# Optimization experiments

Measured on AMD Instinct MI355X. Metric: run time of the kernel, lower is better.

Reference implementation:

```python
import jax, jax.numpy as jnp
import numpy as np

N_OUT = 4096
N_IN = 4096
FRAC_SPARSE = 0.5
N_SPARSE = int(FRAC_SPARSE * N_OUT * N_IN)  # 8388608
TOKENS = 256


def setup_inputs() -> dict:
    key = jax.random.key(0)
    k1, k2 = jax.random.split(key)
    # x: activations fed to F.linear
    x = jax.random.normal(k1, (TOKENS, N_IN), dtype=jnp.float32)
    # sparse_values: nn.Parameter of size n_sparse
    sparse_values = jax.random.normal(k2, (N_SPARSE,), dtype=jnp.float32) * 0.02
    # sparse_mask as sorted unique row-major flat indices of True entries.
    # torch `out[mask] = values` fills values into True positions in row-major
    # order, which equals scattering values at the ascending-sorted flat idxs.
    rng = np.random.default_rng(0)
    flat_idx = np.sort(rng.permutation(N_OUT * N_IN)[:N_SPARSE]).astype(np.int32)
    return {"x": x, "sparse_values": sparse_values, "flat_idx": jnp.asarray(flat_idx)}


def reference(x, sparse_values, flat_idx):
    # reconstruct(): dense [n_out, n_in] weight via scatter of sparse values
    W = (
        jnp.zeros((N_OUT * N_IN,), dtype=sparse_values.dtype)
        .at[flat_idx]
        .set(sparse_values)
        .reshape(N_OUT, N_IN)
    )
    # F.linear(x, W) == x @ W.T
    return x @ W.T
```

## Files before the change

### kernel.cpp

```cpp
#include <hip/hip_runtime.h>
#include <stdint.h>

#define N_OUT    4096
#define N_IN     4096
#define TOKENS   256
#define N_SPARSE 8388608
#define SPLITK   8
#define KCHUNK   256
#define NCHUNK   2
#define NSEG     (N_IN / KCHUNK)
#define CPW      (NSEG + 1)
#define BN       64

typedef __attribute__((ext_vector_type(8))) short bf16x8;
typedef __attribute__((ext_vector_type(8))) unsigned short u16x8;
typedef __attribute__((ext_vector_type(4))) float f32x4;

__device__ __forceinline__ unsigned short f2bf(float f) {
    union { float f; unsigned u; } v; v.f = f;
    unsigned r = v.u + 0x7fffu + ((v.u >> 16) & 1u);
    return (unsigned short)(r >> 16);
}

__device__ __forceinline__ float bf2f(unsigned short u) {
    union { unsigned u; float f; } v; v.u = ((unsigned)u) << 16;
    return v.f;
}

__device__ __forceinline__ void ld4(const int* __restrict__ idx,
                                    const float* __restrict__ vals,
                                    int jb, int4& i4, float4& v4) {
    if (jb + 4 <= N_SPARSE) {
        i4 = *(const int4*)(idx + jb);
        v4 = *(const float4*)(vals + jb);
    } else {
        i4 = int4{0, 0, 0, 0}; v4 = float4{0.f, 0.f, 0.f, 0.f};
        #pragma unroll
        for (int e = 0; e < 4; ++e) {
            const int j = jb + e;
            if (j < N_SPARSE) { (&i4.x)[e] = idx[j]; (&v4.x)[e] = vals[j]; }
        }
    }
}

__device__ __forceinline__ void consume4(const int4& i4, const float4& v4, int jb,
                                         int start, int end, int base,
                                         unsigned short* __restrict__ brow, int rx) {
    #pragma unroll
    for (int e = 0; e < 4; ++e) {
        const int j = jb + e;
        if (j >= start && j < end) {
            const int cc = (&i4.x)[e] - base;
            brow[((cc & ~7) ^ rx) | (cc & 7)] = f2bf((&v4.x)[e]);
        }
    }
}

__global__ void prep(const float* __restrict__ x, const int* __restrict__ idx,
                     unsigned short* __restrict__ xs, int* __restrict__ cp) {
    const int b = blockIdx.x;
    const int t = threadIdx.x;
    if (b < 1024) {
        const int i = (b * 256 + t) * 4;
        const int m = i >> 12;
        const int k = i & 4095;
        const float4 v = *(const float4*)(x + i);
        ushort4 o;
        o.x = f2bf(v.x); o.y = f2bf(v.y); o.z = f2bf(v.z); o.w = f2bf(v.w);
        const int lane = (m & 15) | (((k >> 3) & 3) << 4);
        const int addr = ((k >> 5) * 16 + (m >> 4)) * 512 + lane * 8 + (k & 7);
        *(ushort4*)(xs + addr) = o;
    } else {
        const int e = (b - 1024) * 256 + t;
        const int r = e / CPW;
        const int z = e - r * CPW;
        const int target = r * N_IN + z * KCHUNK;
        int lo = 0, hi = N_SPARSE;
        while (lo < hi) { int m = (lo + hi) >> 1; if (idx[m] < target) lo = m + 1; else hi = m; }
        cp[e] = lo;
    }
}

__global__ __launch_bounds__(512) void fused_gemm(
        const unsigned short* __restrict__ xs,
        const int* __restrict__ idx,
        const float* __restrict__ vals,
        const int* __restrict__ cp,
        unsigned short* __restrict__ part)
{
    __shared__ short Bs[BN * KCHUNK];

    const int tid = threadIdx.x;
    const int l   = tid & 63;
    const int w   = tid >> 6;
    const int bn  = blockIdx.x;
    const int bz  = blockIdx.y;

    const int rl    = tid >> 3;
    const int sub   = tid & 7;
    const int rglob = bn * BN + rl;
    const int rx    = (rl & 7) << 3;
    unsigned short* brow = (unsigned short*)Bs + rl * KCHUNK;

    const int lr  = l & 15;
    const int lkg = l >> 4;
    f32x4 acc[2][4] = {};

    #pragma unroll
    for (int c = 0; c < NCHUNK; ++c) {
        const int seg = bz * NCHUNK + c;

        {
            const u16x8 z8 = {};
            unsigned short* b0 = (unsigned short*)Bs + tid * 32;
            #pragma unroll
            for (int q = 0; q < 4; ++q) *(u16x8*)(b0 + q * 8) = z8;
        }
        __syncthreads();

        {
            const int start = cp[rglob * CPW + seg];
            const int end   = cp[rglob * CPW + seg + 1];
            const int base  = rglob * N_IN + seg * KCHUNK;

            int ja = (start & ~3) + sub * 4;
            int jb_ = ja + 32, jc = ja + 64, jd = ja + 96;
            int4 ia, ib, ic, id; float4 va, vb, vc, vd;
            if (ja  < end) ld4(idx, vals, ja,  ia, va);
            if (jb_ < end) ld4(idx, vals, jb_, ib, vb);
            if (jc  < end) ld4(idx, vals, jc,  ic, vc);
            if (jd  < end) ld4(idx, vals, jd,  id, vd);
            while (ja < end) {
                consume4(ia, va, ja, start, end, base, brow, rx);
                ja += 128; if (ja < end) ld4(idx, vals, ja, ia, va);
                if (jb_ < end) {
                    consume4(ib, vb, jb_, start, end, base, brow, rx);
                    jb_ += 128; if (jb_ < end) ld4(idx, vals, jb_, ib, vb);
                }
                if (jc < end) {
                    consume4(ic, vc, jc, start, end, base, brow, rx);
                    jc += 128; if (jc < end) ld4(idx, vals, jc, ic, vc);
                }
                if (jd < end) {
                    consume4(id, vd, jd, start, end, base, brow, rx);
                    jd += 128; if (jd < end) ld4(idx, vals, jd, id, vd);
                }
            }
        }
        __syncthreads();

        const unsigned short* ax = xs + ((size_t)(seg * 8) * 16) * 512 + l * 8;
        #pragma unroll 2
        for (int kk = 0; kk < KCHUNK / 32; ++kk) {
            bf16x8 af[2], bfr[4];
            #pragma unroll
            for (int i = 0; i < 2; ++i)
                af[i] = *(const bf16x8*)(ax + (size_t)(kk * 16 + w * 2 + i) * 512);
            #pragma unroll
            for (int i = 0; i < 4; ++i) {
                const int n    = i * 16 + lr;
                const int slot = (kk * 4 + lkg) ^ (n & 7);
                bfr[i] = *(const bf16x8*)&Bs[n * KCHUNK + slot * 8];
            }
            #pragma unroll
            for (int mi = 0; mi < 2; ++mi)
                #pragma unroll
                for (int ni = 0; ni < 4; ++ni)
                    acc[mi][ni] = __builtin_amdgcn_mfma_f32_16x16x32_bf16(
                                      af[mi], bfr[ni], acc[mi][ni], 0, 0, 0);
        }
        __syncthreads();
    }

    unsigned short* po = part + (size_t)bz * (TOKENS * N_OUT) + (size_t)bn * BN;
    #pragma unroll
    for (int mi = 0; mi < 2; ++mi)
        #pragma unroll
        for (int r = 0; r < 4; ++r) {
            const int m = w * 32 + mi * 16 + lkg * 4 + r;
            #pragma unroll
            for (int ni = 0; ni < 4; ++ni) {
                const int n = ni * 16 + lr;
                po[(size_t)m * N_OUT + n] = f2bf(acc[mi][ni][r]);
            }
        }
}

__global__ void reduce_k(const unsigned short* __restrict__ part, float* __restrict__ out) {
    const int i = (blockIdx.x * 256 + threadIdx.x) * 8;
    float a[8] = {};
    for (int z = 0; z < SPLITK; ++z) {
        const u16x8 p = *(const u16x8*)(part + (size_t)z * (TOKENS * N_OUT) + i);
        #pragma unroll
        for (int j = 0; j < 8; ++j) a[j] += bf2f((unsigned short)p[j]);
    }
    float4 o0 = { a[0], a[1], a[2], a[3] };
    float4 o1 = { a[4], a[5], a[6], a[7] };
    *(float4*)(out + i)     = o0;
    *(float4*)(out + i + 4) = o1;
}

__global__ void fallback_rowcsr(const float* __restrict__ x, const float* __restrict__ vals,
                                const int* __restrict__ idx, float* __restrict__ out) {
    const int o = blockIdx.x;
    const int t = threadIdx.x;
    __shared__ int   scol[256];
    __shared__ float sval[256];

    int lo = 0, hi = N_SPARSE;
    const int target = o * N_IN;
    while (lo < hi) { int m = (lo + hi) >> 1; if (idx[m] < target) lo = m + 1; else hi = m; }
    const int start = lo;
    hi = N_SPARSE;
    const int target2 = target + N_IN;
    while (lo < hi) { int m = (lo + hi) >> 1; if (idx[m] < target2) lo = m + 1; else hi = m; }
    const int end = lo;

    float acc = 0.f;
    const float* xr = x + (size_t)t * N_IN;
    for (int base = start; base < end; base += 256) {
        const int k = base + t;
        if (k < end) { scol[t] = idx[k] - target; sval[t] = vals[k]; }
        __syncthreads();
        const int cnt = min(256, end - base);
        for (int j = 0; j < cnt; ++j) acc += sval[j] * xr[scol[j]];
        __syncthreads();
    }
    out[(size_t)t * N_OUT + o] = acc;
}

extern "C" void kernel_launch(void* const* d_in, const int* in_sizes, int n_in,
                              void* d_out, int out_size, void* d_ws, size_t ws_size,
                              hipStream_t stream) {
    const float* x    = (const float*)d_in[0];
    const float* vals = (const float*)d_in[1];
    const int*   idx  = (const int*)d_in[2];
    float* out = (float*)d_out;

    const size_t part_bytes = (size_t)SPLITK * TOKENS * N_OUT * 2;
    const size_t xs_bytes   = (size_t)TOKENS * N_IN * 2;
    const size_t cp_bytes   = (size_t)N_OUT * CPW * 4;
    const size_t need = part_bytes + xs_bytes + cp_bytes;

    if (ws_size >= need) {
        unsigned short* part = (unsigned short*)d_ws;
        unsigned short* xs   = (unsigned short*)((char*)d_ws + part_bytes);
        int*            cp   = (int*)((char*)d_ws + part_bytes + xs_bytes);

        prep<<<1024 + (N_OUT * CPW) / 256, 256, 0, stream>>>(x, idx, xs, cp);
        dim3 grid(N_OUT / BN, SPLITK);
        fused_gemm<<<grid, 512, 0, stream>>>(xs, idx, vals, cp, part);
        reduce_k<<<(TOKENS * N_OUT) / 2048, 256, 0, stream>>>(part, out);
    } else {
        fallback_rowcsr<<<N_OUT, TOKENS, 0, stream>>>(x, vals, idx, out);
    }
}
```

Baseline: 45.68 us.

## Prefetch next chunk's sparse loads during MFMA and deepen load pipeline

Manually unrolls the two K-chunks and issues the sparse index/value loads for the second chunk before the MFMA loop of the first, so that global-load latency overlaps compute. Each thread now keeps six in-flight loads with stride 192, up from four with stride 128. The first chunk's loads are also started before LDS zeroing, and launch bounds now request 4 blocks per CU. The extra prefetch registers add pressure, and forcing 4 blocks per CU may cause spills.

```diff
diff --git a/kernel.cpp b/kernel.cpp
--- a/kernel.cpp
+++ b/kernel.cpp
@@ -11,6 +11,7 @@
 #define NSEG     (N_IN / KCHUNK)
 #define CPW      (NSEG + 1)
 #define BN       64
+#define ADV      192
 
 typedef __attribute__((ext_vector_type(8))) short bf16x8;
 typedef __attribute__((ext_vector_type(8))) unsigned short u16x8;
@@ -81,7 +82,7 @@
     }
 }
 
-__global__ __launch_bounds__(512) void fused_gemm(
+__global__ __launch_bounds__(512, 4) void fused_gemm(
         const unsigned short* __restrict__ xs,
         const int* __restrict__ idx,
         const float* __restrict__ vals,
@@ -97,59 +98,57 @@
     const int bz  = blockIdx.y;
 
     const int rl    = tid >> 3;
-    const int sub   = tid & 7;
+    const int sub   = tid & 3;
+    const int sub8  = tid & 7;
     const int rglob = bn * BN + rl;
     const int rx    = (rl & 7) << 3;
     unsigned short* brow = (unsigned short*)Bs + rl * KCHUNK;
 
+    const int seg0 = bz * NCHUNK;
+    const int e0 = cp[rglob * CPW + seg0];
+    const int e1 = cp[rglob * CPW + seg0 + 1];
+    const int e2 = cp[rglob * CPW + seg0 + 2];
+
+    int gstart, gend, gbase, jstart;
+    int  bj0, bj1, bj2, bj3, bj4, bj5;
+    int4 bi0, bi1, bi2, bi3, bi4, bi5;
+    float4 bv0, bv1, bv2, bv3, bv4, bv5;
+
+#define PRO(q) do { bj##q = jstart + q * 32; \
+                    if (bj##q < gend) ld4(idx, vals, bj##q, bi##q, bv##q); } while (0)
+#define STEP(q) do { if (bj##q < gend) { \
+                        consume4(bi##q, bv##q, bj##q, gstart, gend, gbase, brow, rx); \
+                        bj##q += ADV; \
+                        if (bj##q < gend) ld4(idx, vals, bj##q, bi##q, bv##q); } } while (0)
+
+    gstart = e0; gend = e1; gbase = rglob * N_IN + seg0 * KCHUNK;
+    jstart = (gstart & ~3) + sub8 * 4;
+    PRO(0); PRO(1); PRO(2); PRO(3); PRO(4); PRO(5);
+
+    {
+        const u16x8 z8 = {};
+        unsigned short* b0 = (unsigned short*)Bs + tid * 32;
+        #pragma unroll
+        for (int q = 0; q < 4; ++q) *(u16x8*)(b0 + q * 8) = z8;
+    }
+    __syncthreads();
+
+    while (bj0 < gend) { STEP(0); STEP(1); STEP(2); STEP(3); STEP(4); STEP(5); }
+
+    {
+        const int gs1 = e1, ge1 = e2;
+        gstart = gs1; gend = ge1; gbase += KCHUNK;
+        jstart = (gstart & ~3) + sub8 * 4;
+        PRO(0); PRO(1); PRO(2); PRO(3); PRO(4); PRO(5);
+    }
+    __syncthreads();
+
     const int lr  = l & 15;
     const int lkg = l >> 4;
     f32x4 acc[2][4] = {};
 
-    #pragma unroll
-    for (int c = 0; c < NCHUNK; ++c) {
-        const int seg = bz * NCHUNK + c;
-
-        {
-            const u16x8 z8 = {};
-            unsigned short* b0 = (unsigned short*)Bs + tid * 32;
-            #pragma unroll
-            for (int q = 0; q < 4; ++q) *(u16x8*)(b0 + q * 8) = z8;
-        }
-        __syncthreads();
-
-        {
-            const int start = cp[rglob * CPW + seg];
-            const int end   = cp[rglob * CPW + seg + 1];
-            const int base  = rglob * N_IN + seg * KCHUNK;
-
-            int ja = (start & ~3) + sub * 4;
-            int jb_ = ja + 32, jc = ja + 64, jd = ja + 96;
-            int4 ia, ib, ic, id; float4 va, vb, vc, vd;
-            if (ja  < end) ld4(idx, vals, ja,  ia, va);
-            if (jb_ < end) ld4(idx, vals, jb_, ib, vb);
-            if (jc  < end) ld4(idx, vals, jc,  ic, vc);
-            if (jd  < end) ld4(idx, vals, jd,  id, vd);
-            while (ja < end) {
-                consume4(ia, va, ja, start, end, base, brow, rx);
-                ja += 128; if (ja < end) ld4(idx, vals, ja, ia, va);
-                if (jb_ < end) {
-                    consume4(ib, vb, jb_, start, end, base, brow, rx);
-                    jb_ += 128; if (jb_ < end) ld4(idx, vals, jb_, ib, vb);
-                }
-                if (jc < end) {
-                    consume4(ic, vc, jc, start, end, base, brow, rx);
-                    jc += 128; if (jc < end) ld4(idx, vals, jc, ic, vc);
-                }
-                if (jd < end) {
-                    consume4(id, vd, jd, start, end, base, brow, rx);
-                    jd += 128; if (jd < end) ld4(idx, vals, jd, id, vd);
-                }
-            }
-        }
-        __syncthreads();
-
-        const unsigned short* ax = xs + ((size_t)(seg * 8) * 16) * 512 + l * 8;
+    {
+        const unsigned short* ax = xs + (size_t)(seg0 * 8 * 16) * 512 + l * 8;
         #pragma unroll 2
         for (int kk = 0; kk < KCHUNK / 32; ++kk) {
             bf16x8 af[2], bfr[4];
@@ -169,8 +168,44 @@
                     acc[mi][ni] = __builtin_amdgcn_mfma_f32_16x16x32_bf16(
                                       af[mi], bfr[ni], acc[mi][ni], 0, 0, 0);
         }
-        __syncthreads();
-    }
+    }
+    __syncthreads();
+
+    {
+        const u16x8 z8 = {};
+        unsigned short* b0 = (unsigned short*)Bs + tid * 32;
+        #pragma unroll
+        for (int q = 0; q < 4; ++q) *(u16x8*)(b0 + q * 8) = z8;
+    }
+    __syncthreads();
+
+    while (bj0 < gend) { STEP(0); STEP(1); STEP(2); STEP(3); STEP(4); STEP(5); }
+    __syncthreads();
+
+    {
+        const unsigned short* ax = xs + (size_t)((seg0 + 1) * 8 * 16) * 512 + l * 8;
+        #pragma unroll 2
+        for (int kk = 0; kk < KCHUNK / 32; ++kk) {
+            bf16x8 af[2], bfr[4];
+            #pragma unroll
+            for (int i = 0; i < 2; ++i)
+                af[i] = *(const bf16x8*)(ax + (size_t)(kk * 16 + w * 2 + i) * 512);
+            #pragma unroll
+            for (int i = 0; i < 4; ++i) {
+                const int n    = i * 16 + lr;
+                const int slot = (kk * 4 + lkg) ^ (n & 7);
+                bfr[i] = *(const bf16x8*)&Bs[n * KCHUNK + slot * 8];
+            }
+            #pragma unroll
+            for (int mi = 0; mi < 2; ++mi)
+                #pragma unroll
+                for (int ni = 0; ni < 4; ++ni)
+                    acc[mi][ni] = __builtin_amdgcn_mfma_f32_16x16x32_bf16(
+                                      af[mi], bfr[ni], acc[mi][ni], 0, 0, 0);
+        }
+    }
+#undef PRO
+#undef STEP
 
     unsigned short* po = part + (size_t)bz * (TOKENS * N_OUT) + (size_t)bn * BN;
     #pragma unroll
```

Measured after the change: 46.93 us. +2.7%, slower.
